# Kernel tuning notes

Measured on AMD Instinct MI355X. Metric: run time of the kernel, lower is better.

## Reference

```python
import jax, jax.numpy as jnp
import numpy as np

N = 131072

def setup_inputs() -> dict:
    key = jax.random.key(0)
    k_x, k_e, k_w2, k_b2, k_w3, k_b3, k_w4 = jax.random.split(key, 7)
    x = jax.random.randint(k_x, (N, 32), 0, 7424, dtype=jnp.int32)
    emb = jax.random.normal(k_e, (7424, 128), dtype=jnp.float32) * 0.05
    W2 = jax.random.normal(k_w2, (32, 128), dtype=jnp.float32) * 0.05
    b2 = jax.random.normal(k_b2, (32,), dtype=jnp.float32) * 0.05
    W3 = jax.random.normal(k_w3, (32, 64), dtype=jnp.float32) * 0.05
    b3 = jax.random.normal(k_b3, (32,), dtype=jnp.float32) * 0.05
    W4 = jax.random.normal(k_w4, (1, 64), dtype=jnp.float32) * 0.05
    return {"x": x, "emb": emb, "W2": W2, "b2": b2, "W3": W3, "b3": b3, "W4": W4}

def reference(x, emb, W2, b2, W3, b3, W4):
    # x: [N, 32] int indices; use first 29 slots
    idx = x[..., :29]
    h = emb[idx].sum(axis=-2)                    # [N, 128] embedding-bag sum
    h = jax.nn.relu(h)
    h = h @ W2.T + b2                            # [N, 32]
    h = jax.nn.relu(jnp.concatenate((h, -h), axis=-1))   # [N, 64] sign-concat
    h = h @ W3.T + b3                            # [N, 32]
    h = jax.nn.relu(jnp.concatenate((h, -h), axis=-1))   # [N, 64]
    return h @ W4.T                              # [N, 1] (no bias)
```

## Files before the change

kernel.cpp:

```cpp
#include <hip/hip_runtime.h>
#include <hip/hip_fp16.h>


typedef _Float16 h2v_t  __attribute__((ext_vector_type(2)));
typedef _Float16 half8  __attribute__((ext_vector_type(8)));
typedef float    f32x4  __attribute__((ext_vector_type(4)));

constexpr int RPB = 64;

__global__ __launch_bounds__(256) void prep_fp16(
    const float* __restrict__ emb, __half2* __restrict__ emb16,
    const float* __restrict__ W2, const float* __restrict__ W3,
    _Float16* __restrict__ W2h, _Float16* __restrict__ W3h,
    int npairs_real, int npairs_tot, int do_w)
{
    int i = blockIdx.x * blockDim.x + threadIdx.x;
    if (i < npairs_tot) {
        float2 v = make_float2(0.f, 0.f);
        if (i < npairs_real) v = ((const float2*)emb)[i];
        emb16[i] = __floats2half2_rn(v.x, v.y);
    }
    if (do_w) {
        if (i < 4096) W2h[i] = (_Float16)W2[i];
        if (i < 2048) W3h[i] = (_Float16)W3[i];
    }
}

__global__ __launch_bounds__(256, 8) void nnue_one(
    const int*      __restrict__ x,
    const __half*   __restrict__ emb16,
    const _Float16* __restrict__ W2h,
    const _Float16* __restrict__ W3h,
    const float*    __restrict__ b2,
    const float*    __restrict__ b3,
    const float*    __restrict__ W4,
    float*          __restrict__ out, int n)
{
    __shared__ __align__(16) char hmem[4][4096];
    __shared__ __align__(16) char xmem[4][1024];

    const int tid  = threadIdx.x;
    const int lane = tid & 63;
    const int wave = tid >> 6;
    const int row0 = blockIdx.x * RPB;
    const int wrow0 = __builtin_amdgcn_readfirstlane(row0 + wave * 16);

    const int g   = lane >> 4;
    const int sub = lane & 15;
    const unsigned subOff = (unsigned)sub * 16u;

    uint4* hT = (uint4*)&hmem[wave][0];
    unsigned short* xw = (unsigned short*)&xmem[wave][0];

    {
        const int4* xb = (const int4*)(x + (size_t)wrow0 * 32);
        int4 a = xb[lane * 2];
        int4 b = xb[lane * 2 + 1];
        if ((lane & 3) == 3) { b.y = 7424; b.z = 7424; b.w = 7424; }
        uint4 p;
        p.x = ((unsigned)a.x & 0xffffu) | ((unsigned)a.y << 16);
        p.y = ((unsigned)a.z & 0xffffu) | ((unsigned)a.w << 16);
        p.z = ((unsigned)b.x & 0xffffu) | ((unsigned)b.y << 16);
        p.w = ((unsigned)b.z & 0xffffu) | ((unsigned)b.w << 16);
        ((uint4*)xw)[lane] = p;
    }

    #pragma unroll 4
    for (int r = 0; r < 16; ++r) {
        const unsigned short* xrow = xw + r * 32 + g;
        uint4 v[8];
        #pragma unroll
        for (int b = 0; b < 8; ++b) {
            const unsigned idx = xrow[4 * b];
            const unsigned off = (idx << 8) + subOff;
            v[b] = *(const uint4*)((const char*)emb16 + off);
        }
        h2v_t hacc[4];
        #pragma unroll
        for (int q = 0; q < 4; ++q) hacc[q] = (h2v_t)0;
        #pragma unroll
        for (int b = 0; b < 8; ++b) {
            hacc[0] += __builtin_bit_cast(h2v_t, v[b].x);
            hacc[1] += __builtin_bit_cast(h2v_t, v[b].y);
            hacc[2] += __builtin_bit_cast(h2v_t, v[b].z);
            hacc[3] += __builtin_bit_cast(h2v_t, v[b].w);
        }
        #pragma unroll
        for (int q = 0; q < 4; ++q) {
            unsigned u = __builtin_bit_cast(unsigned, hacc[q]);
            h2v_t t = __builtin_bit_cast(h2v_t, u);
            t += __builtin_bit_cast(h2v_t, (unsigned)__shfl_xor((int)u, 16));
            unsigned u2 = __builtin_bit_cast(unsigned, t);
            t += __builtin_bit_cast(h2v_t, (unsigned)__shfl_xor((int)u2, 32));
            hacc[q] = __builtin_elementwise_max(t, (h2v_t)0);
        }
        if (g == 0) {
            uint4 o;
            o.x = __builtin_bit_cast(unsigned, hacc[0]);
            o.y = __builtin_bit_cast(unsigned, hacc[1]);
            o.z = __builtin_bit_cast(unsigned, hacc[2]);
            o.w = __builtin_bit_cast(unsigned, hacc[3]);
            hT[r * 16 + (sub ^ (r & 7))] = o;
        }
    }

    const int q  = lane >> 4;
    const int nn = lane & 15;

    half8 bw2[2][4];
    #pragma unroll
    for (int nt = 0; nt < 2; ++nt)
        #pragma unroll
        for (int kk = 0; kk < 4; ++kk)
            bw2[nt][kk] = __builtin_bit_cast(half8,
                *(const uint4*)((const char*)W2h +
                    ((nt * 16 + nn) * 128 + kk * 32 + q * 8) * 2));

    half8 af[4];
    #pragma unroll
    for (int kk = 0; kk < 4; ++kk)
        af[kk] = __builtin_bit_cast(half8,
            hT[nn * 16 + ((4 * kk + q) ^ (nn & 7))]);

    f32x4 acc0 = {0.f, 0.f, 0.f, 0.f}, acc1 = {0.f, 0.f, 0.f, 0.f};
    #pragma unroll
    for (int kk = 0; kk < 4; ++kk) {
        acc0 = __builtin_amdgcn_mfma_f32_16x16x32_f16(af[kk], bw2[0][kk], acc0, 0, 0, 0);
        acc1 = __builtin_amdgcn_mfma_f32_16x16x32_f16(af[kk], bw2[1][kk], acc1, 0, 0, 0);
    }
    const float bb0 = b2[nn], bb1 = b2[16 + nn];

    _Float16* a2 = (_Float16*)&hmem[wave][0];
    #pragma unroll
    for (int r = 0; r < 4; ++r) {
        const float v0 = acc0[r] + bb0;
        const float v1 = acc1[r] + bb1;
        const int m = q * 4 + r;
        a2[m * 68 + nn]      = (_Float16)fmaxf(v0, 0.f);
        a2[m * 68 + 16 + nn] = (_Float16)fmaxf(v1, 0.f);
        a2[m * 68 + 32 + nn] = (_Float16)fmaxf(-v0, 0.f);
        a2[m * 68 + 48 + nn] = (_Float16)fmaxf(-v1, 0.f);
    }

    half8 bw3[2][2];
    #pragma unroll
    for (int nt = 0; nt < 2; ++nt)
        #pragma unroll
        for (int kk = 0; kk < 2; ++kk)
            bw3[nt][kk] = __builtin_bit_cast(half8,
                *(const uint4*)((const char*)W3h +
                    ((nt * 16 + nn) * 64 + kk * 32 + q * 8) * 2));

    half8 a2f[2];
    #pragma unroll
    for (int kk = 0; kk < 2; ++kk) {
        const _Float16* p = &a2[nn * 68 + kk * 32 + q * 8];
        half8 t;
        #pragma unroll
        for (int j = 0; j < 8; ++j) t[j] = p[j];
        a2f[kk] = t;
    }

    f32x4 acc30 = {0.f, 0.f, 0.f, 0.f}, acc31 = {0.f, 0.f, 0.f, 0.f};
    #pragma unroll
    for (int kk = 0; kk < 2; ++kk) {
        acc30 = __builtin_amdgcn_mfma_f32_16x16x32_f16(a2f[kk], bw3[0][kk], acc30, 0, 0, 0);
        acc31 = __builtin_amdgcn_mfma_f32_16x16x32_f16(a2f[kk], bw3[1][kk], acc31, 0, 0, 0);
    }
    const float bb30 = b3[nn], bb31 = b3[16 + nn];

    const float w4a = W4[nn],      w4b = W4[16 + nn];
    const float w4c = W4[32 + nn], w4d = W4[48 + nn];
    float o[4];
    #pragma unroll
    for (int r = 0; r < 4; ++r) {
        const float v0 = acc30[r] + bb30;
        const float v1 = acc31[r] + bb31;
        o[r] = fmaxf(v0, 0.f) * w4a + fmaxf(-v0, 0.f) * w4c
             + fmaxf(v1, 0.f) * w4b + fmaxf(-v1, 0.f) * w4d;
    }
    #pragma unroll
    for (int s = 1; s < 16; s <<= 1) {
        #pragma unroll
        for (int r = 0; r < 4; ++r) o[r] += __shfl_xor(o[r], s);
    }
    if (nn == 0) {
        #pragma unroll
        for (int r = 0; r < 4; ++r) {
            const int row = wrow0 + q * 4 + r;
            if (row < n) out[row] = o[r];
        }
    }
}

__global__ __launch_bounds__(256) void nnue_fused(
    const int*    __restrict__ x,
    const __half* __restrict__ emb16,
    const float*  __restrict__ W2, const float* __restrict__ b2,
    const float*  __restrict__ W3, const float* __restrict__ b3,
    const float*  __restrict__ W4,
    float*        __restrict__ out, int n)
{
    __shared__ int     xlds[4][512];
    __shared__ __half2 hbuf[64][65];
    __shared__ float   h2T[32 * 64];
    __shared__ float   obuf[4][64];

    const int tid  = threadIdx.x;
    const int lane = tid & 63;
    const int wave = tid >> 6;
    const int row0 = blockIdx.x * RPB;
    const int wrow0 = __builtin_amdgcn_readfirstlane(row0 + wave * 16);
    const int g   = lane >> 4;
    const int sub = lane & 15;
    const unsigned subOff = (unsigned)sub * 16u;

    {
        const int4* xb = (const int4*)(x + (size_t)wrow0 * 32);
        int4 a = xb[lane * 2];
        int4 b = xb[lane * 2 + 1];
        if ((lane & 3) == 3) { b.y = 7424; b.z = 7424; b.w = 7424; }
        ((int4*)&xlds[wave][0])[lane * 2]     = a;
        ((int4*)&xlds[wave][0])[lane * 2 + 1] = b;
    }

    #pragma unroll 4
    for (int r = 0; r < 16; ++r) {
        const int* xrow = &xlds[wave][r * 32 + g];
        uint4 v[8];
        #pragma unroll
        for (int b = 0; b < 8; ++b) {
            const int idx = xrow[4 * b];
            const unsigned off = ((unsigned)idx << 8) + subOff;
            v[b] = *(const uint4*)((const char*)emb16 + off);
        }
        h2v_t hacc[4];
        #pragma unroll
        for (int q = 0; q < 4; ++q) hacc[q] = (h2v_t)0;
        #pragma unroll
        for (int b = 0; b < 8; ++b) {
            hacc[0] += __builtin_bit_cast(h2v_t, v[b].x);
            hacc[1] += __builtin_bit_cast(h2v_t, v[b].y);
            hacc[2] += __builtin_bit_cast(h2v_t, v[b].z);
            hacc[3] += __builtin_bit_cast(h2v_t, v[b].w);
        }
        #pragma unroll
        for (int q = 0; q < 4; ++q) {
            unsigned u = __builtin_bit_cast(unsigned, hacc[q]);
            h2v_t t = __builtin_bit_cast(h2v_t, u);
            t += __builtin_bit_cast(h2v_t, (unsigned)__shfl_xor((int)u, 16));
            unsigned u2 = __builtin_bit_cast(unsigned, t);
            t += __builtin_bit_cast(h2v_t, (unsigned)__shfl_xor((int)u2, 32));
            hacc[q] = __builtin_elementwise_max(t, (h2v_t)0);
        }
        if (g == 0) {
            const int row = wave * 16 + r;
            #pragma unroll
            for (int q = 0; q < 4; ++q)
                hbuf[row][sub * 4 + q] = __builtin_bit_cast(__half2, hacc[q]);
        }
    }
    __syncthreads();

    {
        const int j0 = wave * 8;
        const int rr = lane;
        float acc[8];
        #pragma unroll
        for (int j = 0; j < 8; ++j) acc[j] = b2[j0 + j];
        #pragma unroll
        for (int d2 = 0; d2 < 64; ++d2) {
            const __half2 hv = hbuf[rr][d2];
            const float vx = __low2float(hv), vy = __high2float(hv);
            #pragma unroll
            for (int j = 0; j < 8; ++j) {
                const float* w = W2 + (size_t)(j0 + j) * 128 + d2 * 2;
                acc[j] = fmaf(vx, w[0], acc[j]);
                acc[j] = fmaf(vy, w[1], acc[j]);
            }
        }
        #pragma unroll
        for (int j = 0; j < 8; ++j) h2T[(j0 + j) * 64 + rr] = acc[j];
    }
    __syncthreads();

    {
        const int j0 = wave * 8;
        const int rr = lane;
        float h2v[32];
        #pragma unroll
        for (int k = 0; k < 32; ++k) h2v[k] = h2T[k * 64 + rr];
        float acc[8];
        #pragma unroll
        for (int j = 0; j < 8; ++j) acc[j] = b3[j0 + j];
        #pragma unroll
        for (int k = 0; k < 32; ++k) {
            const float p = fmaxf(h2v[k], 0.f);
            const float m = fmaxf(-h2v[k], 0.f);
            #pragma unroll
            for (int j = 0; j < 8; ++j) {
                const float* w = W3 + (size_t)(j0 + j) * 64;
                acc[j] = fmaf(p, w[k],      acc[j]);
                acc[j] = fmaf(m, w[32 + k], acc[j]);
            }
        }
        float o = 0.f;
        #pragma unroll
        for (int j = 0; j < 8; ++j) {
            const int jj = j0 + j;
            o = fmaf(fmaxf(acc[j], 0.f),  W4[jj],      o);
            o = fmaf(fmaxf(-acc[j], 0.f), W4[32 + jj], o);
        }
        obuf[wave][rr] = o;
    }
    __syncthreads();

    if (tid < 64) {
        const int row = row0 + tid;
        if (row < n)
            out[row] = obuf[0][tid] + obuf[1][tid] + obuf[2][tid] + obuf[3][tid];
    }
}

extern "C" void kernel_launch(void* const* d_in, const int* in_sizes, int n_in,
                              void* d_out, int out_size, void* d_ws, size_t ws_size,
                              hipStream_t stream) {
    const int*   x   = (const int*)  d_in[0];
    const float* emb = (const float*)d_in[1];
    const float* W2  = (const float*)d_in[2];
    const float* b2  = (const float*)d_in[3];
    const float* W3  = (const float*)d_in[4];
    const float* b3  = (const float*)d_in[5];
    const float* W4  = (const float*)d_in[6];
    float* out = (float*)d_out;
    const int n = out_size;

    __half2* emb16 = (__half2*)d_ws;
    const int npairs_real = 7424 * 64;
    const int npairs_tot  = 7425 * 64;

    const size_t emb_bytes = (size_t)7425 * 256;
    const size_t w2h_off   = emb_bytes;
    const size_t w3h_off   = w2h_off + 8192;
    const size_t need      = w3h_off + 4096;
    const bool   fused_ok  = ws_size >= need;

    _Float16* W2h = fused_ok ? (_Float16*)((char*)d_ws + w2h_off) : nullptr;
    _Float16* W3h = fused_ok ? (_Float16*)((char*)d_ws + w3h_off) : nullptr;

    hipLaunchKernelGGL(prep_fp16, dim3((npairs_tot + 255) / 256), dim3(256),
                       0, stream, emb, emb16, W2, W3, W2h, W3h,
                       npairs_real, npairs_tot, fused_ok ? 1 : 0);

    if (fused_ok) {
        hipLaunchKernelGGL(nnue_one, dim3((n + RPB - 1) / RPB), dim3(256),
                           0, stream, x, (const __half*)emb16, W2h, W3h,
                           b2, b3, W4, out, n);
    } else {
        hipLaunchKernelGGL(nnue_fused, dim3((n + RPB - 1) / RPB), dim3(256),
                           0, stream, x, (const __half*)emb16, W2, b2, W3, b3,
                           W4, out, n);
    }
}
```

Measured before the change: 118.2 us.

## Quantize embedding table to int8 with global absmax scale and packed integer gather-sum

Adds an absmax reduction kernel and a prep kernel that quantize the embedding table to biased uint8 with a single global scale. The main kernel gathers half as many bytes per row and accumulates with packed 16-bit integer adds, using byte masks and perm to split even and odd bytes. Lanes are remapped to 8 features per lane, and the result is dequantized to fp16 before the MFMA layers. This cuts gather bandwidth and cache footprint, at the cost of an extra launch, a memset and atomic, and reduced accuracy from 8-bit quantization.

```diff
diff --git a/kernel.cpp b/kernel.cpp
--- a/kernel.cpp
+++ b/kernel.cpp
@@ -8,11 +8,57 @@
 
 constexpr int RPB = 64;
 
+__global__ __launch_bounds__(256) void emb_absmax(
+    const float4* __restrict__ emb4, unsigned* __restrict__ amax, int n4)
+{
+    int i = blockIdx.x * blockDim.x + threadIdx.x;
+    float m = 0.f;
+    if (i < n4) {
+        float4 v = emb4[i];
+        m = fmaxf(fmaxf(fabsf(v.x), fabsf(v.y)), fmaxf(fabsf(v.z), fabsf(v.w)));
+    }
+    #pragma unroll
+    for (int s = 1; s < 64; s <<= 1)
+        m = fmaxf(m, __shfl_xor(m, s));
+    if ((threadIdx.x & 63) == 0)
+        atomicMax(amax, __builtin_bit_cast(unsigned, m));
+}
+
+__global__ __launch_bounds__(256) void prep_q8(
+    const float4* __restrict__ emb4, unsigned* __restrict__ emb8,
+    const float* __restrict__ W2, const float* __restrict__ W3,
+    _Float16* __restrict__ W2h, _Float16* __restrict__ W3h,
+    const unsigned* __restrict__ amax)
+{
+    const int i = blockIdx.x * blockDim.x + threadIdx.x;
+    const float am = __builtin_bit_cast(float, *amax);
+    const float qs = 127.f / am;
+    if (i < 7425 * 32) {
+        unsigned w = 0x80808080u;
+        if (i < 7424 * 32) {
+            float4 v = emb4[i];
+            int q0 = (int)rintf(v.x * qs);
+            int q1 = (int)rintf(v.y * qs);
+            int q2 = (int)rintf(v.z * qs);
+            int q3 = (int)rintf(v.w * qs);
+            q0 = min(127, max(-127, q0));
+            q1 = min(127, max(-127, q1));
+            q2 = min(127, max(-127, q2));
+            q3 = min(127, max(-127, q3));
+            w = (unsigned)(q0 + 128)
+              | ((unsigned)(q2 + 128) << 8)
+              | ((unsigned)(q1 + 128) << 16)
+              | ((unsigned)(q3 + 128) << 24);
+        }
+        emb8[i] = w;
+    }
+    if (i < 4096) W2h[i] = (_Float16)W2[i];
+    if (i < 2048) W3h[i] = (_Float16)W3[i];
+}
+
 __global__ __launch_bounds__(256) void prep_fp16(
     const float* __restrict__ emb, __half2* __restrict__ emb16,
-    const float* __restrict__ W2, const float* __restrict__ W3,
-    _Float16* __restrict__ W2h, _Float16* __restrict__ W3h,
-    int npairs_real, int npairs_tot, int do_w)
+    int npairs_real, int npairs_tot)
 {
     int i = blockIdx.x * blockDim.x + threadIdx.x;
     if (i < npairs_tot) {
@@ -20,20 +66,17 @@
         if (i < npairs_real) v = ((const float2*)emb)[i];
         emb16[i] = __floats2half2_rn(v.x, v.y);
     }
-    if (do_w) {
-        if (i < 4096) W2h[i] = (_Float16)W2[i];
-        if (i < 2048) W3h[i] = (_Float16)W3[i];
-    }
-}
-
-__global__ __launch_bounds__(256, 8) void nnue_one(
+}
+
+__global__ __launch_bounds__(256, 8) void nnue_one_q8(
     const int*      __restrict__ x,
-    const __half*   __restrict__ emb16,
+    const unsigned* __restrict__ emb8,
     const _Float16* __restrict__ W2h,
     const _Float16* __restrict__ W3h,
     const float*    __restrict__ b2,
     const float*    __restrict__ b3,
     const float*    __restrict__ W4,
+    const unsigned* __restrict__ amax,
     float*          __restrict__ out, int n)
 {
     __shared__ __align__(16) char hmem[4][4096];
@@ -45,11 +88,10 @@
     const int row0 = blockIdx.x * RPB;
     const int wrow0 = __builtin_amdgcn_readfirstlane(row0 + wave * 16);
 
-    const int g   = lane >> 4;
-    const int sub = lane & 15;
-    const unsigned subOff = (unsigned)sub * 16u;
-
-    uint4* hT = (uint4*)&hmem[wave][0];
+    const int f = lane >> 3;
+    const int p = lane & 7;
+    const unsigned pOff = (unsigned)p * 16u;
+
     unsigned short* xw = (unsigned short*)&xmem[wave][0];
 
     {
@@ -57,53 +99,71 @@
         int4 a = xb[lane * 2];
         int4 b = xb[lane * 2 + 1];
         if ((lane & 3) == 3) { b.y = 7424; b.z = 7424; b.w = 7424; }
-        uint4 p;
-        p.x = ((unsigned)a.x & 0xffffu) | ((unsigned)a.y << 16);
-        p.y = ((unsigned)a.z & 0xffffu) | ((unsigned)a.w << 16);
-        p.z = ((unsigned)b.x & 0xffffu) | ((unsigned)b.y << 16);
-        p.w = ((unsigned)b.z & 0xffffu) | ((unsigned)b.w << 16);
-        ((uint4*)xw)[lane] = p;
-    }
+        uint4 pk;
+        pk.x = ((unsigned)a.x & 0xffffu) | ((unsigned)a.y << 16);
+        pk.y = ((unsigned)a.z & 0xffffu) | ((unsigned)a.w << 16);
+        pk.z = ((unsigned)b.x & 0xffffu) | ((unsigned)b.y << 16);
+        pk.w = ((unsigned)b.z & 0xffffu) | ((unsigned)b.w << 16);
+        ((uint4*)xw)[lane] = pk;
+    }
+
+    const float am = __builtin_bit_cast(float, *amax);
+    const float sc = am * (1.f / 127.f);
+    const float cb = -4096.f * sc;
 
     #pragma unroll 4
     for (int r = 0; r < 16; ++r) {
-        const unsigned short* xrow = xw + r * 32 + g;
-        uint4 v[8];
-        #pragma unroll
-        for (int b = 0; b < 8; ++b) {
-            const unsigned idx = xrow[4 * b];
-            const unsigned off = (idx << 8) + subOff;
-            v[b] = *(const uint4*)((const char*)emb16 + off);
-        }
-        h2v_t hacc[4];
-        #pragma unroll
-        for (int q = 0; q < 4; ++q) hacc[q] = (h2v_t)0;
-        #pragma unroll
-        for (int b = 0; b < 8; ++b) {
-            hacc[0] += __builtin_bit_cast(h2v_t, v[b].x);
-            hacc[1] += __builtin_bit_cast(h2v_t, v[b].y);
-            hacc[2] += __builtin_bit_cast(h2v_t, v[b].z);
-            hacc[3] += __builtin_bit_cast(h2v_t, v[b].w);
-        }
-        #pragma unroll
-        for (int q = 0; q < 4; ++q) {
-            unsigned u = __builtin_bit_cast(unsigned, hacc[q]);
-            h2v_t t = __builtin_bit_cast(h2v_t, u);
-            t += __builtin_bit_cast(h2v_t, (unsigned)__shfl_xor((int)u, 16));
-            unsigned u2 = __builtin_bit_cast(unsigned, t);
-            t += __builtin_bit_cast(h2v_t, (unsigned)__shfl_xor((int)u2, 32));
-            hacc[q] = __builtin_elementwise_max(t, (h2v_t)0);
-        }
-        if (g == 0) {
-            uint4 o;
-            o.x = __builtin_bit_cast(unsigned, hacc[0]);
-            o.y = __builtin_bit_cast(unsigned, hacc[1]);
-            o.z = __builtin_bit_cast(unsigned, hacc[2]);
-            o.w = __builtin_bit_cast(unsigned, hacc[3]);
-            hT[r * 16 + (sub ^ (r & 7))] = o;
-        }
-    }
-
+        const unsigned short* xrow = xw + r * 32 + f;
+        uint4 v[4];
+        #pragma unroll
+        for (int b = 0; b < 4; ++b) {
+            const unsigned idx = xrow[8 * b];
+            v[b] = *(const uint4*)((const char*)emb8 + ((idx << 7) + pOff));
+        }
+        unsigned aL0 = 0, aL1 = 0, aL2 = 0, aL3 = 0;
+        unsigned aH0 = 0, aH1 = 0, aH2 = 0, aH3 = 0;
+        #pragma unroll
+        for (int b = 0; b < 4; ++b) {
+            aL0 += v[b].x & 0x00ff00ffu;
+            aL1 += v[b].y & 0x00ff00ffu;
+            aL2 += v[b].z & 0x00ff00ffu;
+            aL3 += v[b].w & 0x00ff00ffu;
+            aH0 += __builtin_amdgcn_perm(0u, v[b].x, 0x0c030c01u);
+            aH1 += __builtin_amdgcn_perm(0u, v[b].y, 0x0c030c01u);
+            aH2 += __builtin_amdgcn_perm(0u, v[b].z, 0x0c030c01u);
+            aH3 += __builtin_amdgcn_perm(0u, v[b].w, 0x0c030c01u);
+        }
+        #pragma unroll
+        for (int s = 8; s < 64; s <<= 1) {
+            aL0 += (unsigned)__shfl_xor((int)aL0, s);
+            aL1 += (unsigned)__shfl_xor((int)aL1, s);
+            aL2 += (unsigned)__shfl_xor((int)aL2, s);
+            aL3 += (unsigned)__shfl_xor((int)aL3, s);
+            aH0 += (unsigned)__shfl_xor((int)aH0, s);
+            aH1 += (unsigned)__shfl_xor((int)aH1, s);
+            aH2 += (unsigned)__shfl_xor((int)aH2, s);
+            aH3 += (unsigned)__shfl_xor((int)aH3, s);
+        }
+        unsigned sl  = (f & 1) ? aL1 : aL0;
+        unsigned sl2 = (f & 1) ? aL3 : aL2;
+        sl = (f & 2) ? sl2 : sl;
+        unsigned sh  = (f & 1) ? aH1 : aH0;
+        unsigned sh2 = (f & 1) ? aH3 : aH2;
+        sh = (f & 2) ? sh2 : sh;
+        const unsigned w = (f & 4) ? sh : sl;
+        const int pi   = ((f & 3) << 1) | (f >> 2);
+        const int wIdx = p * 8 + pi;
+        float f0 = (float)(w & 0xffffu) * sc + cb;
+        float f1 = (float)(w >> 16)     * sc + cb;
+        h2v_t hv;
+        hv[0] = (_Float16)fmaxf(f0, 0.f);
+        hv[1] = (_Float16)fmaxf(f1, 0.f);
+        const int byteOff = r * 256
+                          + ((((wIdx >> 2) ^ (r & 7)) << 4) | ((wIdx & 3) << 2));
+        *(unsigned*)(&hmem[wave][byteOff]) = __builtin_bit_cast(unsigned, hv);
+    }
+
+    const uint4* hT = (const uint4*)&hmem[wave][0];
     const int q  = lane >> 4;
     const int nn = lane & 15;
 
@@ -154,10 +214,10 @@
     half8 a2f[2];
     #pragma unroll
     for (int kk = 0; kk < 2; ++kk) {
-        const _Float16* p = &a2[nn * 68 + kk * 32 + q * 8];
+        const _Float16* pp = &a2[nn * 68 + kk * 32 + q * 8];
         half8 t;
         #pragma unroll
-        for (int j = 0; j < 8; ++j) t[j] = p[j];
+        for (int j = 0; j < 8; ++j) t[j] = pp[j];
         a2f[kk] = t;
     }
 
@@ -295,13 +355,13 @@
         for (int j = 0; j < 8; ++j) acc[j] = b3[j0 + j];
         #pragma unroll
         for (int k = 0; k < 32; ++k) {
-            const float p = fmaxf(h2v[k], 0.f);
-            const float m = fmaxf(-h2v[k], 0.f);
+            const float pz = fmaxf(h2v[k], 0.f);
+            const float mz = fmaxf(-h2v[k], 0.f);
             #pragma unroll
             for (int j = 0; j < 8; ++j) {
                 const float* w = W3 + (size_t)(j0 + j) * 64;
-                acc[j] = fmaf(p, w[k],      acc[j]);
-                acc[j] = fmaf(m, w[32 + k], acc[j]);
+                acc[j] = fmaf(pz, w[k],      acc[j]);
+                acc[j] = fmaf(mz, w[32 + k], acc[j]);
             }
         }
         float o = 0.f;
@@ -335,28 +395,38 @@
     float* out = (float*)d_out;
     const int n = out_size;
 
-    __half2* emb16 = (__half2*)d_ws;
-    const int npairs_real = 7424 * 64;
-    const int npairs_tot  = 7425 * 64;
-
-    const size_t emb_bytes = (size_t)7425 * 256;
-    const size_t w2h_off   = emb_bytes;
-    const size_t w3h_off   = w2h_off + 8192;
-    const size_t need      = w3h_off + 4096;
-    const bool   fused_ok  = ws_size >= need;
-
-    _Float16* W2h = fused_ok ? (_Float16*)((char*)d_ws + w2h_off) : nullptr;
-    _Float16* W3h = fused_ok ? (_Float16*)((char*)d_ws + w3h_off) : nullptr;
-
-    hipLaunchKernelGGL(prep_fp16, dim3((npairs_tot + 255) / 256), dim3(256),
-                       0, stream, emb, emb16, W2, W3, W2h, W3h,
-                       npairs_real, npairs_tot, fused_ok ? 1 : 0);
-
-    if (fused_ok) {
-        hipLaunchKernelGGL(nnue_one, dim3((n + RPB - 1) / RPB), dim3(256),
-                           0, stream, x, (const __half*)emb16, W2h, W3h,
-                           b2, b3, W4, out, n);
+    const size_t emb8_bytes = (size_t)7425 * 128;
+    const size_t w2h_off    = emb8_bytes;
+    const size_t w3h_off    = w2h_off + 8192;
+    const size_t amax_off   = w3h_off + 4096;
+    const size_t need_q8    = amax_off + 16;
+
+    if (ws_size >= need_q8) {
+        unsigned* emb8  = (unsigned*)d_ws;
+        _Float16* W2h   = (_Float16*)((char*)d_ws + w2h_off);
+        _Float16* W3h   = (_Float16*)((char*)d_ws + w3h_off);
+        unsigned* amax  = (unsigned*)((char*)d_ws + amax_off);
+
+        hipMemsetAsync(amax, 0, 4, stream);
+
+        const int n4 = 7424 * 32;
+        hipLaunchKernelGGL(emb_absmax, dim3((n4 + 255) / 256), dim3(256),
+                           0, stream, (const float4*)emb, amax, n4);
+
+        const int nq = 7425 * 32;
+        hipLaunchKernelGGL(prep_q8, dim3((nq + 255) / 256), dim3(256),
+                           0, stream, (const float4*)emb, emb8, W2, W3,
+                           W2h, W3h, amax);
+
+        hipLaunchKernelGGL(nnue_one_q8, dim3((n + RPB - 1) / RPB), dim3(256),
+                           0, stream, x, emb8, W2h, W3h, b2, b3, W4, amax,
+                           out, n);
     } else {
+        __half2* emb16 = (__half2*)d_ws;
+        const int npairs_real = 7424 * 64;
+        const int npairs_tot  = 7425 * 64;
+        hipLaunchKernelGGL(prep_fp16, dim3((npairs_tot + 255) / 256), dim3(256),
+                           0, stream, emb, emb16, npairs_real, npairs_tot);
         hipLaunchKernelGGL(nnue_fused, dim3((n + RPB - 1) / RPB), dim3(256),
                            0, stream, x, (const __half*)emb16, W2, b2, W3, b3,
                            W4, out, n);
```

Result: slower. 168.4 us (+42.4%).
